# Performance work log

Measured on AMD Instinct MI355X. Metric: run time of the kernel, lower is better.

Reference implementation:

```python
import jax, jax.numpy as jnp
import numpy as np

N_EMBED = 1024
N_HEAD = 16
HEAD_SIZE = N_EMBED // N_HEAD
LN_EPS = 1e-5


def setup_inputs() -> dict:
    key = jax.random.key(0)
    ks = jax.random.split(key, 12)
    B, T, C = 8, 1024, N_EMBED
    s = 0.02
    return {
        "x": jax.random.normal(ks[0], (B, T, C), dtype=jnp.float32),
        "Wq": jax.random.normal(ks[1], (C, C), dtype=jnp.float32) * s,
        "Wk": jax.random.normal(ks[2], (C, C), dtype=jnp.float32) * s,
        "Wv": jax.random.normal(ks[3], (C, C), dtype=jnp.float32) * s,
        "Wp": jax.random.normal(ks[4], (C, C), dtype=jnp.float32) * s,
        "bp": jnp.zeros((C,), dtype=jnp.float32),
        "ln1_g": jnp.ones((C,), dtype=jnp.float32),
        "ln1_b": jnp.zeros((C,), dtype=jnp.float32),
        "ln2_g": jnp.ones((C,), dtype=jnp.float32),
        "ln2_b": jnp.zeros((C,), dtype=jnp.float32),
        "W1": jax.random.normal(ks[5], (C, 4 * C), dtype=jnp.float32) * s,
        "b1": jnp.zeros((4 * C,), dtype=jnp.float32),
        "W2": jax.random.normal(ks[6], (4 * C, C), dtype=jnp.float32) * s,
        "b2": jnp.zeros((C,), dtype=jnp.float32),
    }


def _layernorm(x, g, b):
    mu = jnp.mean(x, axis=-1, keepdims=True)
    var = jnp.mean(jnp.square(x - mu), axis=-1, keepdims=True)
    return (x - mu) * jax.lax.rsqrt(var + LN_EPS) * g + b


def _block(x, Wq, Wk, Wv, Wp, bp, ln1_g, ln1_b, ln2_g, ln2_b, W1, b1, W2, b2):
    B, T, C = x.shape
    H, D = N_HEAD, HEAD_SIZE
    xn = _layernorm(x, ln1_g, ln1_b)
    # fused QKV for all heads (heads concatenated along feature dim, same as torch cat)
    q = (xn @ Wq).reshape(B, T, H, D)
    k = (xn @ Wk).reshape(B, T, H, D)
    v = (xn @ Wv).reshape(B, T, H, D)
    scores = jnp.einsum("bthd,bshd->bhts", q, k) / jnp.sqrt(jnp.float32(D))
    causal = jnp.tril(jnp.ones((T, T), dtype=bool))
    scores = jnp.where(causal, scores, jnp.float32(-jnp.inf))
    wei = jax.nn.softmax(scores, axis=-1)  # dropout = identity (eval)
    attn = jnp.einsum("bhts,bshd->bthd", wei, v).reshape(B, T, C)
    sa_out = attn @ Wp + bp  # dropout = identity (eval)
    x = x + sa_out
    xn2 = _layernorm(x, ln2_g, ln2_b)
    ff = jax.nn.relu(xn2 @ W1 + b1) @ W2 + b2  # dropout = identity (eval)
    return x + ff


def reference(x, Wq, Wk, Wv, Wp, bp, ln1_g, ln1_b, ln2_g, ln2_b, W1, b1, W2, b2):
    return _block(x, Wq, Wk, Wv, Wp, bp, ln1_g, ln1_b, ln2_g, ln2_b, W1, b1, W2, b2)
```

## Files before the change

kernel.cpp:

```cpp
#include <hip/hip_runtime.h>
#include <cstdint>
#include <cstddef>

using u16 = unsigned short;
typedef __attribute__((ext_vector_type(8))) short bh8;
typedef __attribute__((ext_vector_type(4))) float f4;

__device__ __forceinline__ u16 f2bf(float f) {
    union { float f; uint32_t u; } c; c.f = f;
    uint32_t u = c.u;
    u += 0x7FFFu + ((u >> 16) & 1u);
    return (u16)(u >> 16);
}

__device__ __forceinline__ void gload16(const void* g, void* l) {
    __builtin_amdgcn_global_load_lds(
        (__attribute__((address_space(1))) void*)g,
        (__attribute__((address_space(3))) void*)l,
        16, 0, 0);
}

__device__ __forceinline__ f4 mfma16(bh8 a, bh8 b, f4 c) {
    return __builtin_amdgcn_mfma_f32_16x16x32_bf16(a, b, c, 0, 0, 0);
}

__global__ __launch_bounds__(256) void wconv_kernel(
    const float* __restrict__ W, u16* __restrict__ Wt, int K, int N)
{
    __shared__ float t[32][33];
    const int tx = threadIdx.x & 31, ty = threadIdx.x >> 5;
    const int n0 = blockIdx.x * 32, k0 = blockIdx.y * 32;
#pragma unroll
    for (int j = 0; j < 4; ++j)
        t[ty + 8 * j][tx] = W[(size_t)(k0 + ty + 8 * j) * N + n0 + tx];
    __syncthreads();
#pragma unroll
    for (int j = 0; j < 4; ++j)
        Wt[(size_t)(n0 + ty + 8 * j) * K + k0 + tx] = f2bf(t[tx][ty + 8 * j]);
}

__global__ __launch_bounds__(256) void ln_kernel(
    const float* __restrict__ x, const float* __restrict__ g,
    const float* __restrict__ b, u16* __restrict__ out)
{
    const int row = blockIdx.x;
    const int tid = threadIdx.x;
    const float4 v = ((const float4*)(x + (size_t)row * 1024))[tid];
    float s  = v.x + v.y + v.z + v.w;
    float sq = v.x * v.x + v.y * v.y + v.z * v.z + v.w * v.w;
#pragma unroll
    for (int m = 1; m < 64; m <<= 1) {
        s  += __shfl_xor(s, m);
        sq += __shfl_xor(sq, m);
    }
    __shared__ float red[8];
    const int w = tid >> 6;
    if ((tid & 63) == 0) { red[w * 2] = s; red[w * 2 + 1] = sq; }
    __syncthreads();
    s  = red[0] + red[2] + red[4] + red[6];
    sq = red[1] + red[3] + red[5] + red[7];
    const float mu   = s * (1.0f / 1024.0f);
    const float var  = sq * (1.0f / 1024.0f) - mu * mu;
    const float rstd = rsqrtf(var + 1e-5f);
    const float4 gv = ((const float4*)g)[tid];
    const float4 bv = ((const float4*)b)[tid];
    ushort4 o;
    o.x = f2bf((v.x - mu) * rstd * gv.x + bv.x);
    o.y = f2bf((v.y - mu) * rstd * gv.y + bv.y);
    o.z = f2bf((v.z - mu) * rstd * gv.z + bv.z);
    o.w = f2bf((v.w - mu) * rstd * gv.w + bv.w);
    ((ushort4*)(out + (size_t)row * 1024))[tid] = o;
}

__global__ __launch_bounds__(256) void vtrans_kernel(
    const u16* __restrict__ vb, u16* __restrict__ vtb)
{
    __shared__ u16 t[64][66];
    const int bh = blockIdx.y;
    const int t0 = blockIdx.x * 64;
    const int b = bh >> 4, h = bh & 15;
    const u16* src = vb + (size_t)b * 1024 * 1024 + h * 64;
    const int rs = threadIdx.x >> 3, cs = threadIdx.x & 7;
#pragma unroll
    for (int it = 0; it < 2; ++it) {
        const int r = it * 32 + rs;
        *(uint4*)&t[r][cs * 8] = *(const uint4*)(src + (size_t)(t0 + r) * 1024 + cs * 8);
    }
    __syncthreads();
    u16* dst = vtb + (size_t)bh * 65536 + t0;
#pragma unroll
    for (int it = 0; it < 2; ++it) {
        const int d = it * 32 + rs;
        u16 tmp[8];
#pragma unroll
        for (int j = 0; j < 8; ++j) tmp[j] = t[cs * 8 + j][d];
        *(uint4*)(dst + (size_t)d * 1024 + cs * 8) = *(const uint4*)tmp;
    }
}

template <int NF, int EPI>
__global__ __launch_bounds__(512) void gemm8_kernel(
    const u16* __restrict__ A, const u16* __restrict__ Bt,
    int M, int N, int K,
    const float* __restrict__ bias, const float* __restrict__ resid,
    float* __restrict__ outf, u16* __restrict__ outb)
{
    constexpr int BN = NF * 64;
    __shared__ u16 Al[3][256 * 32];
    __shared__ u16 Bl[3][BN * 32];

    const int tid  = threadIdx.x;
    const int lane = tid & 63;
    const int w    = tid >> 6;
    const int wr   = w >> 2;
    const int wc   = w & 3;
    const int lrow = lane & 15;
    const int lg   = lane >> 4;

    const int gx  = gridDim.x;
    const int nwg = gx * gridDim.y;
    const int lin = blockIdx.y * gx + blockIdx.x;
    const int swz = (lin & 7) * (nwg >> 3) + (lin >> 3);
    const int nt  = swz % gx, mt = swz / gx;

    const int NT = K >> 5;

    auto stageA = [&](int slot, int kt) {
#pragma unroll
        for (int it = 0; it < 2; ++it) {
            const int r = it * 128 + (tid >> 2);
            gload16(A + (size_t)(mt * 256 + r) * K + kt * 32 + (((tid & 3) ^ ((r >> 1) & 3)) << 3),
                    (char*)Al[slot] + it * 8192 + tid * 16);
        }
    };
    auto stageB = [&](int slot, int kt) {
#pragma unroll
        for (int it = 0; it < NF / 2; ++it) {
            const int r = it * 128 + (tid >> 2);
            gload16(Bt + (size_t)(nt * BN + r) * K + kt * 32 + (((tid & 3) ^ ((r >> 1) & 3)) << 3),
                    (char*)Bl[slot] + it * 8192 + tid * 16);
        }
    };

    f4 acc[8][NF] = {};
    bh8 af[8];
    bh8 bf[NF];

    auto readFrags = [&](int slot) {
#pragma unroll
        for (int fm = 0; fm < 8; ++fm) {
            const int R = wr * 128 + fm * 16 + lrow;
            af[fm] = *(const bh8*)&Al[slot][R * 32 + ((lg ^ ((R >> 1) & 3)) << 3)];
        }
#pragma unroll
        for (int fn = 0; fn < NF; ++fn) {
            const int R = wc * (NF * 16) + fn * 16 + lrow;
            bf[fn] = *(const bh8*)&Bl[slot][R * 32 + ((lg ^ ((R >> 1) & 3)) << 3)];
        }
    };
    auto mfmaHalf = [&](int mh) {
#pragma unroll
        for (int fm = 0; fm < 4; ++fm)
#pragma unroll
            for (int fn = 0; fn < NF; ++fn)
                acc[mh * 4 + fm][fn] = mfma16(af[mh * 4 + fm], bf[fn], acc[mh * 4 + fm][fn]);
    };

    stageA(0, 0); stageB(0, 0);
    stageA(1, 1); stageB(1, 1);
    if (NF == 4) asm volatile("s_waitcnt vmcnt(4)" ::: "memory");
    else         asm volatile("s_waitcnt vmcnt(3)" ::: "memory");
    __builtin_amdgcn_s_barrier();
    __builtin_amdgcn_sched_barrier(0);

    int rs3 = 0, ws3 = 2;
    for (int t = 0; t < NT; ++t) {
        const bool pf = (t + 2 < NT);
        readFrags(rs3);
        if (pf) stageA(ws3, t + 2);
        __builtin_amdgcn_s_barrier();
        asm volatile("s_waitcnt lgkmcnt(0)" ::: "memory");
        __builtin_amdgcn_sched_barrier(0);
        __builtin_amdgcn_s_setprio(1);
        mfmaHalf(0);
        __builtin_amdgcn_s_setprio(0);
        __builtin_amdgcn_s_barrier();
        __builtin_amdgcn_sched_barrier(0);
        if (pf) stageB(ws3, t + 2);
        __builtin_amdgcn_s_barrier();
        __builtin_amdgcn_sched_barrier(0);
        __builtin_amdgcn_s_setprio(1);
        mfmaHalf(1);
        __builtin_amdgcn_s_setprio(0);
        if (pf) {
            if (NF == 4) asm volatile("s_waitcnt vmcnt(4)" ::: "memory");
            else         asm volatile("s_waitcnt vmcnt(3)" ::: "memory");
        } else {
            asm volatile("s_waitcnt vmcnt(0)" ::: "memory");
        }
        __builtin_amdgcn_s_barrier();
        __builtin_amdgcn_sched_barrier(0);
        if (++rs3 == 3) rs3 = 0;
        if (++ws3 == 3) ws3 = 0;
    }

    const int r0 = mt * 256 + wr * 128 + lg * 4;
    const int c0 = nt * BN + wc * (NF * 16) + lrow;
#pragma unroll
    for (int fn = 0; fn < NF; ++fn) {
        const int col = c0 + fn * 16;
        const float bvl = (EPI == 1 || EPI == 2) ? bias[col] : 0.0f;
#pragma unroll
        for (int fm = 0; fm < 8; ++fm) {
#pragma unroll
            for (int i = 0; i < 4; ++i) {
                const int rr = r0 + fm * 16 + i;
                const float v = acc[fm][fn][i];
                if (EPI == 1) {
                    const size_t idx = (size_t)rr * N + col;
                    outf[idx] = resid[idx] + v + bvl;
                } else if (EPI == 2) {
                    outb[(size_t)rr * N + col] = f2bf(fmaxf(v + bvl, 0.0f));
                } else {
                    outb[(size_t)(col >> 10) * 8388608 + (size_t)rr * 1024 + (col & 1023)]
                        = f2bf(v);
                }
            }
        }
    }
}

__global__ __launch_bounds__(256, 3) void attn_kernel(
    const u16* __restrict__ Q, const u16* __restrict__ K,
    const u16* __restrict__ Vt, u16* __restrict__ O)
{
    __shared__ u16 Kl[2][64 * 64];
    __shared__ u16 Vl[2][64 * 64];
    __shared__ u16 Pl[4][16 * 72];

    const int tid  = threadIdx.x;
    const int lane = tid & 63;
    const int w    = tid >> 6;
    const int bh   = blockIdx.y;
    const size_t base  = (size_t)(bh >> 4) * (1024 * 1024) + (bh & 15) * 64;
    const size_t vbase = (size_t)bh * 65536;
    const int lrow = lane & 15;
    const int lg   = lane >> 4;
    const int lkb  = lg * 8;
    const int rs   = tid >> 3, cs = tid & 7;

    const u16* Kp = K + base;
    const u16* Vp = Vt + vbase;

#pragma unroll 1
    for (int p = 0; p < 2; ++p) {
        const int qt = p ? (15 - blockIdx.x) : blockIdx.x;
        const int q0 = qt * 64;

        const bh8 aq0 = *(const bh8*)(Q + base + (size_t)(q0 + w * 16 + lrow) * 1024 + lkb);
        const bh8 aq1 = *(const bh8*)(Q + base + (size_t)(q0 + w * 16 + lrow) * 1024 + 32 + lkb);

        f4 o[4] = {};
        float mi[4], li[4];
#pragma unroll
        for (int i = 0; i < 4; ++i) { mi[i] = -__builtin_inff(); li[i] = 0.0f; }

#pragma unroll
        for (int it = 0; it < 2; ++it) {
            const int r = it * 32 + rs;
            gload16(Kp + (size_t)r * 1024 + ((cs ^ (r & 7)) * 8),
                    (char*)Kl[0] + it * 4096 + tid * 16);
            gload16(Vp + (size_t)r * 1024 + ((cs ^ (r & 7)) * 8),
                    (char*)Vl[0] + it * 4096 + tid * 16);
        }
        __syncthreads();

        for (int t = 0; t <= qt; ++t) {
            const int cur = t & 1;
            if (t < qt) {
                const int s1 = (t + 1) * 64;
#pragma unroll
                for (int it = 0; it < 2; ++it) {
                    const int r = it * 32 + rs;
                    gload16(Kp + (size_t)(s1 + r) * 1024 + ((cs ^ (r & 7)) * 8),
                            (char*)Kl[cur ^ 1] + it * 4096 + tid * 16);
                    gload16(Vp + (size_t)r * 1024 + s1 + ((cs ^ (r & 7)) * 8),
                            (char*)Vl[cur ^ 1] + it * 4096 + tid * 16);
                }
            }

            f4 sc[4] = {};
#pragma unroll
            for (int ks = 0; ks < 2; ++ks) {
                const bh8 a = ks ? aq1 : aq0;
#pragma unroll
                for (int fn = 0; fn < 4; ++fn) {
                    const int R = fn * 16 + lrow;
                    const bh8 bk = *(const bh8*)&Kl[cur][R * 64 + ((((ks << 2) + lg) ^ (R & 7)) * 8)];
                    sc[fn] = mfma16(a, bk, sc[fn]);
                }
            }
            const bool diag = (t == qt);
#pragma unroll
            for (int fn = 0; fn < 4; ++fn)
#pragma unroll
                for (int i = 0; i < 4; ++i) {
                    float v = sc[fn][i] * 0.125f;
                    if (diag) {
                        const int r = lg * 4 + i;
                        const int c = fn * 16 + lrow;
                        if (c > w * 16 + r) v = -__builtin_inff();
                    }
                    sc[fn][i] = v;
                }
#pragma unroll
            for (int i = 0; i < 4; ++i) {
                float pm = fmaxf(fmaxf(sc[0][i], sc[1][i]), fmaxf(sc[2][i], sc[3][i]));
#pragma unroll
                for (int m = 1; m < 16; m <<= 1) pm = fmaxf(pm, __shfl_xor(pm, m));
                const float mn   = fmaxf(mi[i], pm);
                const float corr = __expf(mi[i] - mn);
                float rsum = 0.0f;
#pragma unroll
                for (int fn = 0; fn < 4; ++fn) {
                    const float pv = __expf(sc[fn][i] - mn);
                    sc[fn][i] = pv;
                    rsum += pv;
                }
#pragma unroll
                for (int m = 1; m < 16; m <<= 1) rsum += __shfl_xor(rsum, m);
                li[i] = li[i] * corr + rsum;
                mi[i] = mn;
#pragma unroll
                for (int fn = 0; fn < 4; ++fn) o[fn][i] *= corr;
            }
#pragma unroll
            for (int fn = 0; fn < 4; ++fn)
#pragma unroll
                for (int i = 0; i < 4; ++i)
                    Pl[w][(lg * 4 + i) * 72 + fn * 16 + lrow] = f2bf(sc[fn][i]);
#pragma unroll
            for (int ss = 0; ss < 2; ++ss) {
                const bh8 ap = *(const bh8*)&Pl[w][lrow * 72 + ss * 32 + lkb];
#pragma unroll
                for (int fn = 0; fn < 4; ++fn) {
                    const int R = fn * 16 + lrow;
                    const bh8 bv = *(const bh8*)&Vl[cur][R * 64 + ((((ss << 2) + lg) ^ (R & 7)) * 8)];
                    o[fn] = mfma16(ap, bv, o[fn]);
                }
            }
            __syncthreads();
        }

#pragma unroll
        for (int fn = 0; fn < 4; ++fn)
#pragma unroll
            for (int i = 0; i < 4; ++i) {
                const int r = q0 + w * 16 + lg * 4 + i;
                const int c = fn * 16 + lrow;
                O[base + (size_t)r * 1024 + c] = f2bf(o[fn][i] / li[i]);
            }
    }
}

extern "C" void kernel_launch(void* const* d_in, const int* in_sizes, int n_in,
                              void* d_out, int out_size, void* d_ws, size_t ws_size,
                              hipStream_t stream) {
    const float* x    = (const float*)d_in[0];
    const float* Wq   = (const float*)d_in[1];
    const float* Wk   = (const float*)d_in[2];
    const float* Wv   = (const float*)d_in[3];
    const float* Wp   = (const float*)d_in[4];
    const float* bp   = (const float*)d_in[5];
    const float* ln1g = (const float*)d_in[6];
    const float* ln1b = (const float*)d_in[7];
    const float* ln2g = (const float*)d_in[8];
    const float* ln2b = (const float*)d_in[9];
    const float* W1   = (const float*)d_in[10];
    const float* b1   = (const float*)d_in[11];
    const float* W2   = (const float*)d_in[12];
    const float* b2   = (const float*)d_in[13];
    float* out = (float*)d_out;

    u16* ws   = (u16*)d_ws;
    u16* wqkt = ws;
    u16* wpt  = wqkt + (3u << 20);
    u16* w1t  = wpt  + (1u << 20);
    u16* w2t  = w1t  + (4u << 20);
    u16* qb   = w2t  + (4u << 20);
    u16* kb   = qb   + (8u << 20);
    u16* vb   = kb   + (8u << 20);
    u16* xnb  = vb   + (8u << 20);
    u16* vtb  = xnb;
    u16* aob  = vb;
    u16* xn2b = qb;
    u16* h1b  = kb;

    dim3 blk(256);
    wconv_kernel<<<dim3(32, 32),  blk, 0, stream>>>(Wq, wqkt,              1024, 1024);
    wconv_kernel<<<dim3(32, 32),  blk, 0, stream>>>(Wk, wqkt + (1u << 20), 1024, 1024);
    wconv_kernel<<<dim3(32, 32),  blk, 0, stream>>>(Wv, wqkt + (2u << 20), 1024, 1024);
    wconv_kernel<<<dim3(32, 32),  blk, 0, stream>>>(Wp, wpt, 1024, 1024);
    wconv_kernel<<<dim3(128, 32), blk, 0, stream>>>(W1, w1t, 1024, 4096);
    wconv_kernel<<<dim3(32, 128), blk, 0, stream>>>(W2, w2t, 4096, 1024);

    ln_kernel<<<8192, blk, 0, stream>>>(x, ln1g, ln1b, xnb);

    gemm8_kernel<4, 3><<<dim3(12, 32), 512, 0, stream>>>(xnb, wqkt, 8192, 3072, 1024,
                                                         nullptr, nullptr, nullptr, qb);

    vtrans_kernel<<<dim3(16, 128), blk, 0, stream>>>(vb, vtb);

    attn_kernel<<<dim3(8, 128), blk, 0, stream>>>(qb, kb, vtb, aob);

    gemm8_kernel<2, 1><<<dim3(8, 32), 512, 0, stream>>>(aob, wpt, 8192, 1024, 1024,
                                                        bp, x, out, nullptr);

    ln_kernel<<<8192, blk, 0, stream>>>(out, ln2g, ln2b, xn2b);

    gemm8_kernel<4, 2><<<dim3(16, 32), 512, 0, stream>>>(xn2b, w1t, 8192, 4096, 1024,
                                                         b1, nullptr, nullptr, h1b);
    gemm8_kernel<2, 1><<<dim3(8, 32), 512, 0, stream>>>(h1b, w2t, 8192, 1024, 4096,
                                                        b2, out, out, nullptr);
}
```

Baseline: 398.1 us.

## Generalize GEMM warp layout and use split-K with atomics for FFN down-projection

The GEMM kernel is templated on warp-row count and tile width, and gains a z-grid split-K dimension with a per-split K range. The FFN down-projection now uses 256-wide tiles split across two K halves, with results added atomically into the output that already holds the residual; only the first split adds the bias. This aims to raise tile reuse while keeping enough workgroups to fill the device. The cost is float atomic traffic on the output and a summation order that is no longer deterministic. Other launches keep equivalent tile shapes.

After: 424.3 us. 6.6% more time.

```diff
diff --git a/kernel.cpp b/kernel.cpp
--- a/kernel.cpp
+++ b/kernel.cpp
@@ -98,32 +98,37 @@
     }
 }
 
-template <int NF, int EPI>
+template <int MW, int BN, int EPI>
 __global__ __launch_bounds__(512) void gemm8_kernel(
     const u16* __restrict__ A, const u16* __restrict__ Bt,
-    int M, int N, int K,
+    int M, int N, int K, int KT,
     const float* __restrict__ bias, const float* __restrict__ resid,
     float* __restrict__ outf, u16* __restrict__ outb)
 {
-    constexpr int BN = NF * 64;
+    constexpr int NW  = 8 / MW;
+    constexpr int AFR = 16 / MW;
+    constexpr int BFR = BN / NW / 16;
+    constexpr int L   = 2 + BN / 128;
     __shared__ u16 Al[3][256 * 32];
     __shared__ u16 Bl[3][BN * 32];
 
     const int tid  = threadIdx.x;
     const int lane = tid & 63;
     const int w    = tid >> 6;
-    const int wr   = w >> 2;
-    const int wc   = w & 3;
+    const int wr   = w / NW;
+    const int wc   = w % NW;
     const int lrow = lane & 15;
     const int lg   = lane >> 4;
 
-    const int gx  = gridDim.x;
-    const int nwg = gx * gridDim.y;
-    const int lin = blockIdx.y * gx + blockIdx.x;
+    const int gx  = gridDim.x, gy = gridDim.y;
+    const int nwg = gx * gy * gridDim.z;
+    const int lin = (blockIdx.z * gy + blockIdx.y) * gx + blockIdx.x;
     const int swz = (lin & 7) * (nwg >> 3) + (lin >> 3);
-    const int nt  = swz % gx, mt = swz / gx;
-
-    const int NT = K >> 5;
+    const int nt  = swz % gx;
+    const int tmq = swz / gx;
+    const int mt  = tmq % gy;
+    const int kz  = tmq / gy;
+    const int kb  = kz * KT;
 
     auto stageA = [&](int slot, int kt) {
 #pragma unroll
@@ -135,49 +140,50 @@
     };
     auto stageB = [&](int slot, int kt) {
 #pragma unroll
-        for (int it = 0; it < NF / 2; ++it) {
+        for (int it = 0; it < BN / 128; ++it) {
             const int r = it * 128 + (tid >> 2);
             gload16(Bt + (size_t)(nt * BN + r) * K + kt * 32 + (((tid & 3) ^ ((r >> 1) & 3)) << 3),
                     (char*)Bl[slot] + it * 8192 + tid * 16);
         }
     };
 
-    f4 acc[8][NF] = {};
-    bh8 af[8];
-    bh8 bf[NF];
+    f4 acc[AFR][BFR] = {};
+    bh8 af[AFR];
+    bh8 bf[BFR];
 
     auto readFrags = [&](int slot) {
 #pragma unroll
-        for (int fm = 0; fm < 8; ++fm) {
-            const int R = wr * 128 + fm * 16 + lrow;
+        for (int fm = 0; fm < AFR; ++fm) {
+            const int R = wr * (AFR * 16) + fm * 16 + lrow;
             af[fm] = *(const bh8*)&Al[slot][R * 32 + ((lg ^ ((R >> 1) & 3)) << 3)];
         }
 #pragma unroll
-        for (int fn = 0; fn < NF; ++fn) {
-            const int R = wc * (NF * 16) + fn * 16 + lrow;
+        for (int fn = 0; fn < BFR; ++fn) {
+            const int R = wc * (BFR * 16) + fn * 16 + lrow;
             bf[fn] = *(const bh8*)&Bl[slot][R * 32 + ((lg ^ ((R >> 1) & 3)) << 3)];
         }
     };
     auto mfmaHalf = [&](int mh) {
 #pragma unroll
-        for (int fm = 0; fm < 4; ++fm)
-#pragma unroll
-            for (int fn = 0; fn < NF; ++fn)
-                acc[mh * 4 + fm][fn] = mfma16(af[mh * 4 + fm], bf[fn], acc[mh * 4 + fm][fn]);
+        for (int fm = 0; fm < AFR / 2; ++fm)
+#pragma unroll
+            for (int fn = 0; fn < BFR; ++fn)
+                acc[mh * (AFR / 2) + fm][fn] =
+                    mfma16(af[mh * (AFR / 2) + fm], bf[fn], acc[mh * (AFR / 2) + fm][fn]);
     };
 
-    stageA(0, 0); stageB(0, 0);
-    stageA(1, 1); stageB(1, 1);
-    if (NF == 4) asm volatile("s_waitcnt vmcnt(4)" ::: "memory");
-    else         asm volatile("s_waitcnt vmcnt(3)" ::: "memory");
+    stageA(0, kb); stageB(0, kb);
+    stageA(1, kb + 1); stageB(1, kb + 1);
+    if constexpr (L == 4) asm volatile("s_waitcnt vmcnt(4)" ::: "memory");
+    else                  asm volatile("s_waitcnt vmcnt(3)" ::: "memory");
     __builtin_amdgcn_s_barrier();
     __builtin_amdgcn_sched_barrier(0);
 
     int rs3 = 0, ws3 = 2;
-    for (int t = 0; t < NT; ++t) {
-        const bool pf = (t + 2 < NT);
+    for (int t = 0; t < KT; ++t) {
+        const bool pf = (t + 2 < KT);
         readFrags(rs3);
-        if (pf) stageA(ws3, t + 2);
+        if (pf) stageA(ws3, kb + t + 2);
         __builtin_amdgcn_s_barrier();
         asm volatile("s_waitcnt lgkmcnt(0)" ::: "memory");
         __builtin_amdgcn_sched_barrier(0);
@@ -186,15 +192,15 @@
         __builtin_amdgcn_s_setprio(0);
         __builtin_amdgcn_s_barrier();
         __builtin_amdgcn_sched_barrier(0);
-        if (pf) stageB(ws3, t + 2);
+        if (pf) stageB(ws3, kb + t + 2);
         __builtin_amdgcn_s_barrier();
         __builtin_amdgcn_sched_barrier(0);
         __builtin_amdgcn_s_setprio(1);
         mfmaHalf(1);
         __builtin_amdgcn_s_setprio(0);
         if (pf) {
-            if (NF == 4) asm volatile("s_waitcnt vmcnt(4)" ::: "memory");
-            else         asm volatile("s_waitcnt vmcnt(3)" ::: "memory");
+            if constexpr (L == 4) asm volatile("s_waitcnt vmcnt(4)" ::: "memory");
+            else                  asm volatile("s_waitcnt vmcnt(3)" ::: "memory");
         } else {
             asm volatile("s_waitcnt vmcnt(0)" ::: "memory");
         }
@@ -204,14 +210,16 @@
         if (++ws3 == 3) ws3 = 0;
     }
 
-    const int r0 = mt * 256 + wr * 128 + lg * 4;
-    const int c0 = nt * BN + wc * (NF * 16) + lrow;
-#pragma unroll
-    for (int fn = 0; fn < NF; ++fn) {
+    const int r0 = mt * 256 + wr * (AFR * 16) + lg * 4;
+    const int c0 = nt * BN + wc * (BFR * 16) + lrow;
+#pragma unroll
+    for (int fn = 0; fn < BFR; ++fn) {
         const int col = c0 + fn * 16;
-        const float bvl = (EPI == 1 || EPI == 2) ? bias[col] : 0.0f;
-#pragma unroll
-        for (int fm = 0; fm < 8; ++fm) {
+        float bvl = 0.0f;
+        if (EPI == 1 || EPI == 2) bvl = bias[col];
+        if (EPI == 4 && kz == 0)  bvl = bias[col];
+#pragma unroll
+        for (int fm = 0; fm < AFR; ++fm) {
 #pragma unroll
             for (int i = 0; i < 4; ++i) {
                 const int rr = r0 + fm * 16 + i;
@@ -221,9 +229,11 @@
                     outf[idx] = resid[idx] + v + bvl;
                 } else if (EPI == 2) {
                     outb[(size_t)rr * N + col] = f2bf(fmaxf(v + bvl, 0.0f));
-                } else {
+                } else if (EPI == 3) {
                     outb[(size_t)(col >> 10) * 8388608 + (size_t)rr * 1024 + (col & 1023)]
                         = f2bf(v);
+                } else {
+                    atomicAdd(&outf[(size_t)rr * N + col], v + bvl);
                 }
             }
         }
@@ -406,20 +416,21 @@
 
     ln_kernel<<<8192, blk, 0, stream>>>(x, ln1g, ln1b, xnb);
 
-    gemm8_kernel<4, 3><<<dim3(12, 32), 512, 0, stream>>>(xnb, wqkt, 8192, 3072, 1024,
-                                                         nullptr, nullptr, nullptr, qb);
+    gemm8_kernel<2, 256, 3><<<dim3(12, 32, 1), 512, 0, stream>>>(
+        xnb, wqkt, 8192, 3072, 1024, 32, nullptr, nullptr, nullptr, qb);
 
     vtrans_kernel<<<dim3(16, 128), blk, 0, stream>>>(vb, vtb);
 
     attn_kernel<<<dim3(8, 128), blk, 0, stream>>>(qb, kb, vtb, aob);
 
-    gemm8_kernel<2, 1><<<dim3(8, 32), 512, 0, stream>>>(aob, wpt, 8192, 1024, 1024,
-                                                        bp, x, out, nullptr);
+    gemm8_kernel<4, 128, 1><<<dim3(8, 32, 1), 512, 0, stream>>>(
+        aob, wpt, 8192, 1024, 1024, 32, bp, x, out, nullptr);
 
     ln_kernel<<<8192, blk, 0, stream>>>(out, ln2g, ln2b, xn2b);
 
-    gemm8_kernel<4, 2><<<dim3(16, 32), 512, 0, stream>>>(xn2b, w1t, 8192, 4096, 1024,
-                                                         b1, nullptr, nullptr, h1b);
-    gemm8_kernel<2, 1><<<dim3(8, 32), 512, 0, stream>>>(h1b, w2t, 8192, 1024, 4096,
-                                                        b2, out, out, nullptr);
-}
+    gemm8_kernel<2, 256, 2><<<dim3(16, 32, 1), 512, 0, stream>>>(
+        xn2b, w1t, 8192, 4096, 1024, 32, b1, nullptr, nullptr, h1b);
+
+    gemm8_kernel<2, 256, 4><<<dim3(4, 32, 2), 512, 0, stream>>>(
+        h1b, w2t, 8192, 1024, 4096, 64, b2, nullptr, out, nullptr);
+}
```

## Use 64-wide K tiles with double buffering and split-K atomics for W2 GEMM

Applied to the files above, without the earlier changes.

The GEMM kernel now stages 64-element K tiles in two LDS buffers instead of 32-element tiles in three, with a wider XOR swizzle and loads split into half-tiles interleaved with the MFMA phases. This halves the number of barrier-separated iterations. The final FFN down-projection switches to 256-wide N tiles with a 2-way split-K over the grid z dimension, accumulating into the output with float atomicAdd on top of the residual already stored there. The goal is better occupancy and parallelism for the small-N, long-K GEMM, at the cost of atomic traffic and non-deterministic summation order.

Result: slower. 408.1 us (+2.5%).

```diff
diff --git a/kernel.cpp b/kernel.cpp
--- a/kernel.cpp
+++ b/kernel.cpp
@@ -101,13 +101,13 @@
 template <int NF, int EPI>
 __global__ __launch_bounds__(512) void gemm8_kernel(
     const u16* __restrict__ A, const u16* __restrict__ Bt,
-    int M, int N, int K,
+    int M, int N, int K, int KT,
     const float* __restrict__ bias, const float* __restrict__ resid,
     float* __restrict__ outf, u16* __restrict__ outb)
 {
     constexpr int BN = NF * 64;
-    __shared__ u16 Al[3][256 * 32];
-    __shared__ u16 Bl[3][BN * 32];
+    __shared__ u16 Al[2][256 * 64];
+    __shared__ u16 Bl[2][BN * 64];
 
     const int tid  = threadIdx.x;
     const int lane = tid & 63;
@@ -117,28 +117,30 @@
     const int lrow = lane & 15;
     const int lg   = lane >> 4;
 
-    const int gx  = gridDim.x;
-    const int nwg = gx * gridDim.y;
-    const int lin = blockIdx.y * gx + blockIdx.x;
+    const int gx  = gridDim.x, gy = gridDim.y;
+    const int nwg = gx * gy * gridDim.z;
+    const int lin = (blockIdx.z * gy + blockIdx.y) * gx + blockIdx.x;
     const int swz = (lin & 7) * (nwg >> 3) + (lin >> 3);
-    const int nt  = swz % gx, mt = swz / gx;
-
-    const int NT = K >> 5;
-
-    auto stageA = [&](int slot, int kt) {
+    const int nt  = swz % gx;
+    const int tmq = swz / gx;
+    const int mt  = tmq % gy;
+    const int kz  = tmq / gy;
+    const int kb  = kz * KT;
+
+    auto stageA = [&](int slot, int h, int kt) {
 #pragma unroll
         for (int it = 0; it < 2; ++it) {
-            const int r = it * 128 + (tid >> 2);
-            gload16(A + (size_t)(mt * 256 + r) * K + kt * 32 + (((tid & 3) ^ ((r >> 1) & 3)) << 3),
-                    (char*)Al[slot] + it * 8192 + tid * 16);
+            const int r = h * 128 + it * 64 + (tid >> 3);
+            gload16(A + (size_t)(mt * 256 + r) * K + kt * 64 + (((tid & 7) ^ (r & 7)) << 3),
+                    (char*)Al[slot] + (h * 128 + it * 64) * 128 + tid * 16);
         }
     };
-    auto stageB = [&](int slot, int kt) {
+    auto stageB = [&](int slot, int h, int kt) {
 #pragma unroll
         for (int it = 0; it < NF / 2; ++it) {
-            const int r = it * 128 + (tid >> 2);
-            gload16(Bt + (size_t)(nt * BN + r) * K + kt * 32 + (((tid & 3) ^ ((r >> 1) & 3)) << 3),
-                    (char*)Bl[slot] + it * 8192 + tid * 16);
+            const int r = h * (BN / 2) + it * 64 + (tid >> 3);
+            gload16(Bt + (size_t)(nt * BN + r) * K + kt * 64 + (((tid & 7) ^ (r & 7)) << 3),
+                    (char*)Bl[slot] + (h * (BN / 2) + it * 64) * 128 + tid * 16);
         }
     };
 
@@ -146,16 +148,16 @@
     bh8 af[8];
     bh8 bf[NF];
 
-    auto readFrags = [&](int slot) {
+    auto readFrags = [&](int slot, int ks) {
 #pragma unroll
         for (int fm = 0; fm < 8; ++fm) {
             const int R = wr * 128 + fm * 16 + lrow;
-            af[fm] = *(const bh8*)&Al[slot][R * 32 + ((lg ^ ((R >> 1) & 3)) << 3)];
+            af[fm] = *(const bh8*)&Al[slot][R * 64 + ((((ks << 2) + lg) ^ (R & 7)) << 3)];
         }
 #pragma unroll
         for (int fn = 0; fn < NF; ++fn) {
             const int R = wc * (NF * 16) + fn * 16 + lrow;
-            bf[fn] = *(const bh8*)&Bl[slot][R * 32 + ((lg ^ ((R >> 1) & 3)) << 3)];
+            bf[fn] = *(const bh8*)&Bl[slot][R * 64 + ((((ks << 2) + lg) ^ (R & 7)) << 3)];
         }
     };
     auto mfmaHalf = [&](int mh) {
@@ -166,18 +168,17 @@
                 acc[mh * 4 + fm][fn] = mfma16(af[mh * 4 + fm], bf[fn], acc[mh * 4 + fm][fn]);
     };
 
-    stageA(0, 0); stageB(0, 0);
-    stageA(1, 1); stageB(1, 1);
-    if (NF == 4) asm volatile("s_waitcnt vmcnt(4)" ::: "memory");
-    else         asm volatile("s_waitcnt vmcnt(3)" ::: "memory");
+    stageA(0, 0, kb); stageA(0, 1, kb); stageB(0, 0, kb); stageB(0, 1, kb);
+    stageA(1, 0, kb + 1);
+    asm volatile("s_waitcnt vmcnt(2)" ::: "memory");
     __builtin_amdgcn_s_barrier();
     __builtin_amdgcn_sched_barrier(0);
 
-    int rs3 = 0, ws3 = 2;
-    for (int t = 0; t < NT; ++t) {
-        const bool pf = (t + 2 < NT);
-        readFrags(rs3);
-        if (pf) stageA(ws3, t + 2);
+    auto doTile = [&](int t, int s) {
+        const bool pf1 = (t + 1 < KT);
+        const bool pf2 = (t + 2 < KT);
+        readFrags(s, 0);
+        if (pf1) stageA(s ^ 1, 1, kb + t + 1);
         __builtin_amdgcn_s_barrier();
         asm volatile("s_waitcnt lgkmcnt(0)" ::: "memory");
         __builtin_amdgcn_sched_barrier(0);
@@ -186,30 +187,46 @@
         __builtin_amdgcn_s_setprio(0);
         __builtin_amdgcn_s_barrier();
         __builtin_amdgcn_sched_barrier(0);
-        if (pf) stageB(ws3, t + 2);
+        if (pf1) stageB(s ^ 1, 0, kb + t + 1);
         __builtin_amdgcn_s_barrier();
         __builtin_amdgcn_sched_barrier(0);
         __builtin_amdgcn_s_setprio(1);
         mfmaHalf(1);
         __builtin_amdgcn_s_setprio(0);
-        if (pf) {
-            if (NF == 4) asm volatile("s_waitcnt vmcnt(4)" ::: "memory");
-            else         asm volatile("s_waitcnt vmcnt(3)" ::: "memory");
-        } else {
-            asm volatile("s_waitcnt vmcnt(0)" ::: "memory");
-        }
-        __builtin_amdgcn_s_barrier();
-        __builtin_amdgcn_sched_barrier(0);
-        if (++rs3 == 3) rs3 = 0;
-        if (++ws3 == 3) ws3 = 0;
-    }
+        __builtin_amdgcn_s_barrier();
+        __builtin_amdgcn_sched_barrier(0);
+        readFrags(s, 1);
+        if (pf1) stageB(s ^ 1, 1, kb + t + 1);
+        __builtin_amdgcn_s_barrier();
+        asm volatile("s_waitcnt lgkmcnt(0)" ::: "memory");
+        __builtin_amdgcn_sched_barrier(0);
+        __builtin_amdgcn_s_setprio(1);
+        mfmaHalf(0);
+        __builtin_amdgcn_s_setprio(0);
+        __builtin_amdgcn_s_barrier();
+        __builtin_amdgcn_sched_barrier(0);
+        if (pf2) stageA(s, 0, kb + t + 2);
+        __builtin_amdgcn_s_barrier();
+        __builtin_amdgcn_sched_barrier(0);
+        __builtin_amdgcn_s_setprio(1);
+        mfmaHalf(1);
+        __builtin_amdgcn_s_setprio(0);
+        if (pf2) asm volatile("s_waitcnt vmcnt(2)" ::: "memory");
+        else     asm volatile("s_waitcnt vmcnt(0)" ::: "memory");
+        __builtin_amdgcn_s_barrier();
+        __builtin_amdgcn_sched_barrier(0);
+    };
+
+    for (int t = 0; t < KT; t += 2) { doTile(t, 0); doTile(t + 1, 1); }
 
     const int r0 = mt * 256 + wr * 128 + lg * 4;
     const int c0 = nt * BN + wc * (NF * 16) + lrow;
 #pragma unroll
     for (int fn = 0; fn < NF; ++fn) {
         const int col = c0 + fn * 16;
-        const float bvl = (EPI == 1 || EPI == 2) ? bias[col] : 0.0f;
+        float bvl = 0.0f;
+        if (EPI == 1 || EPI == 2) bvl = bias[col];
+        if (EPI == 4 && kz == 0)  bvl = bias[col];
 #pragma unroll
         for (int fm = 0; fm < 8; ++fm) {
 #pragma unroll
@@ -221,9 +238,11 @@
                     outf[idx] = resid[idx] + v + bvl;
                 } else if (EPI == 2) {
                     outb[(size_t)rr * N + col] = f2bf(fmaxf(v + bvl, 0.0f));
-                } else {
+                } else if (EPI == 3) {
                     outb[(size_t)(col >> 10) * 8388608 + (size_t)rr * 1024 + (col & 1023)]
                         = f2bf(v);
+                } else {
+                    atomicAdd(&outf[(size_t)rr * N + col], v + bvl);
                 }
             }
         }
@@ -406,20 +425,21 @@
 
     ln_kernel<<<8192, blk, 0, stream>>>(x, ln1g, ln1b, xnb);
 
-    gemm8_kernel<4, 3><<<dim3(12, 32), 512, 0, stream>>>(xnb, wqkt, 8192, 3072, 1024,
-                                                         nullptr, nullptr, nullptr, qb);
+    gemm8_kernel<4, 3><<<dim3(12, 32, 1), 512, 0, stream>>>(
+        xnb, wqkt, 8192, 3072, 1024, 16, nullptr, nullptr, nullptr, qb);
 
     vtrans_kernel<<<dim3(16, 128), blk, 0, stream>>>(vb, vtb);
 
     attn_kernel<<<dim3(8, 128), blk, 0, stream>>>(qb, kb, vtb, aob);
 
-    gemm8_kernel<2, 1><<<dim3(8, 32), 512, 0, stream>>>(aob, wpt, 8192, 1024, 1024,
-                                                        bp, x, out, nullptr);
+    gemm8_kernel<2, 1><<<dim3(8, 32, 1), 512, 0, stream>>>(
+        aob, wpt, 8192, 1024, 1024, 16, bp, x, out, nullptr);
 
     ln_kernel<<<8192, blk, 0, stream>>>(out, ln2g, ln2b, xn2b);
 
-    gemm8_kernel<4, 2><<<dim3(16, 32), 512, 0, stream>>>(xn2b, w1t, 8192, 4096, 1024,
-                                                         b1, nullptr, nullptr, h1b);
-    gemm8_kernel<2, 1><<<dim3(8, 32), 512, 0, stream>>>(h1b, w2t, 8192, 1024, 4096,
-                                                        b2, out, out, nullptr);
-}
+    gemm8_kernel<4, 2><<<dim3(16, 32, 1), 512, 0, stream>>>(
+        xn2b, w1t, 8192, 4096, 1024, 16, b1, nullptr, nullptr, h1b);
+
+    gemm8_kernel<4, 4><<<dim3(4, 32, 2), 512, 0, stream>>>(
+        h1b, w2t, 8192, 1024, 4096, 32, b2, nullptr, out, nullptr);
+}
```
